# Performance work log

Hardware: AMD Instinct MI355X
Metric: run time of the kernel (lower is better)

Reference implementation:

```python
import jax, jax.numpy as jnp
import numpy as np


def setup_inputs() -> dict:
    key = jax.random.key(0)
    k1, k2 = jax.random.split(key)
    x = jax.random.normal(k1, (32, 128, 128, 128), dtype=jnp.float32)
    conv_w = jax.random.normal(k2, (1, 2, 7, 7), dtype=jnp.float32) * 0.1
    return {"x": x, "conv_w": conv_w}


def reference(x, conv_w):
    # x: [B, C, H, W]; conv_w: [1, 2, 7, 7]
    max_out = jnp.max(x, axis=1, keepdims=True)   # [B,1,H,W]
    avg_out = jnp.mean(x, axis=1, keepdims=True)  # [B,1,H,W]
    stacked = jnp.concatenate([avg_out, max_out], axis=1)  # [B,2,H,W]
    attn = jax.lax.conv_general_dilated(
        stacked, conv_w,
        window_strides=(1, 1), padding=((3, 3), (3, 3)),
        dimension_numbers=("NCHW", "OIHW", "NCHW"),
    )  # [B,1,H,W]
    return x * jax.nn.sigmoid(attn)
```

## Files before the change

kernel.cpp:

```cpp
#include <hip/hip_runtime.h>

#define BB 32
#define CC 128
#define HH 128
#define WW 128
#define HWSZ (HH * WW)
#define CHW (CC * HWSZ)
#define S4 (HWSZ / 4)
#define RPB 8
#define HALO 14

typedef float vfloat4 __attribute__((ext_vector_type(4)));

__device__ __forceinline__ vfloat4 fmax4(vfloat4 a, vfloat4 b) {
    vfloat4 r;
    r.x = fmaxf(a.x, b.x);
    r.y = fmaxf(a.y, b.y);
    r.z = fmaxf(a.z, b.z);
    r.w = fmaxf(a.w, b.w);
    return r;
}

__global__ __launch_bounds__(256, 2) void sa_onepass(
    const float* __restrict__ x, const float* __restrict__ cw,
    float* __restrict__ out) {
    __shared__ float m_lds[2][HALO][WW];
    __shared__ float sig_lds[RPB][WW];
    __shared__ float wsh[2 * 49];

    const int tid = threadIdx.x;
    const int wg  = blockIdx.x;
    const int xcd = wg & 7;
    const int lin = wg >> 3;
    const int b   = xcd * 4 + (lin >> 4);
    const int hb  = lin & 15;
    const int h0  = hb * RPB;

    if (tid < 98) wsh[tid] = cw[tid];

    const int r0 = tid >> 5;
    const int w4 = tid & 31;
    const float* xb = x + (size_t)b * CHW;

    const bool actB = (r0 < HALO - 8);
    const int gh_a = h0 - 3 + r0;
    const int gh_b = h0 - 3 + r0 + 8;
    const bool okA = (gh_a >= 0) && (gh_a < HH);
    const bool okB = actB && (gh_b < HH);
    const int cha = gh_a < 0 ? 0 : (gh_a > HH - 1 ? HH - 1 : gh_a);
    const int chb = gh_b > HH - 1 ? HH - 1 : gh_b;

    const vfloat4* pA = (const vfloat4*)(xb + cha * WW) + w4;
    const vfloat4* pB = (const vfloat4*)(xb + chb * WW) + w4;

    vfloat4 sumA, mxA;
    {
        vfloat4 v = pA[0];
        sumA = v; mxA = v;
    }
    #pragma unroll 8
    for (int c = 1; c < CC; ++c) {
        vfloat4 v = pA[(size_t)c * S4];
        sumA += v;
        mxA = fmax4(mxA, v);
    }
    vfloat4 sumB = {0.f, 0.f, 0.f, 0.f}, mxB = sumB;
    if (actB) {
        vfloat4 v = pB[0];
        sumB = v; mxB = v;
        #pragma unroll 8
        for (int c = 1; c < CC; ++c) {
            vfloat4 t = pB[(size_t)c * S4];
            sumB += t;
            mxB = fmax4(mxB, t);
        }
    }

    const float invC = 1.0f / (float)CC;
    {
        vfloat4 avgA = sumA * invC;
        if (!okA) { avgA = (vfloat4){0,0,0,0}; mxA = (vfloat4){0,0,0,0}; }
        *(vfloat4*)&m_lds[0][r0][w4 * 4] = avgA;
        *(vfloat4*)&m_lds[1][r0][w4 * 4] = mxA;
        if (actB) {
            vfloat4 avgB = sumB * invC;
            if (!okB) { avgB = (vfloat4){0,0,0,0}; mxB = (vfloat4){0,0,0,0}; }
            *(vfloat4*)&m_lds[0][r0 + 8][w4 * 4] = avgB;
            *(vfloat4*)&m_lds[1][r0 + 8][w4 * 4] = mxB;
        }
    }
    __syncthreads();

    {
        const int q = tid >> 7;
        const int w = tid & 127;
        float attn[4] = {0.f, 0.f, 0.f, 0.f};
        #pragma unroll
        for (int ic = 0; ic < 2; ++ic) {
            #pragma unroll
            for (int L = 0; L < 10; ++L) {
                const float* row = &m_lds[ic][q * 4 + L][0];
                #pragma unroll
                for (int kw = 0; kw < 7; ++kw) {
                    int wi = w - 3 + kw;
                    float v = (wi >= 0 && wi < WW) ? row[wi] : 0.0f;
                    #pragma unroll
                    for (int j = 0; j < 4; ++j) {
                        const int kh = L - j;
                        if (kh >= 0 && kh <= 6)
                            attn[j] = fmaf(v, wsh[ic * 49 + kh * 7 + kw], attn[j]);
                    }
                }
            }
        }
        #pragma unroll
        for (int j = 0; j < 4; ++j)
            sig_lds[q * 4 + j][w] = 1.0f / (1.0f + __expf(-attn[j]));
    }
    __syncthreads();

    {
        vfloat4 sig = *(const vfloat4*)&sig_lds[r0][w4 * 4];
        const int s = (h0 + r0) * WW + w4 * 4;
        const vfloat4* px = (const vfloat4*)xb + (s >> 2);
        vfloat4* po = (vfloat4*)(out + (size_t)b * CHW) + (s >> 2);
        #pragma unroll 1
        for (int c0 = CC - 8; c0 >= 0; c0 -= 8) {
            vfloat4 v[8];
            #pragma unroll
            for (int j = 0; j < 8; ++j)
                v[j] = px[(size_t)(c0 + 7 - j) * S4];
            #pragma unroll
            for (int j = 0; j < 8; ++j) {
                vfloat4 o = v[j] * sig;
                __builtin_nontemporal_store(o, po + (size_t)(c0 + 7 - j) * S4);
            }
        }
    }
}

extern "C" void kernel_launch(void* const* d_in, const int* in_sizes, int n_in,
                              void* d_out, int out_size, void* d_ws, size_t ws_size,
                              hipStream_t stream) {
    const float* x  = (const float*)d_in[0];
    const float* cw = (const float*)d_in[1];
    float* out = (float*)d_out;

    sa_onepass<<<BB * (HH / RPB), 256, 0, stream>>>(x, cw, out);
}
```

Baseline: 141.1 us.

## Split fused kernel into reduce-conv kernel and grid-stride multiply kernel

Splits the single-pass kernel into two. The first computes the channel mean/max, runs the 7x7 conv and writes the sigmoid map to workspace. The second is a flat grid-stride kernel that multiplies x by the broadcast sigmoid map, iterating in reverse order so it can reuse x still in cache. This trades the fused design's locality for better occupancy and parallelism in the multiply phase, at the cost of an extra launch, a workspace round trip and re-reading x from memory.

```diff
diff --git a/kernel.cpp b/kernel.cpp
--- a/kernel.cpp
+++ b/kernel.cpp
@@ -21,11 +21,10 @@
     return r;
 }
 
-__global__ __launch_bounds__(256, 2) void sa_onepass(
+__global__ __launch_bounds__(256, 2) void kA_reduce_conv(
     const float* __restrict__ x, const float* __restrict__ cw,
-    float* __restrict__ out) {
+    float* __restrict__ sig) {
     __shared__ float m_lds[2][HALO][WW];
-    __shared__ float sig_lds[RPB][WW];
     __shared__ float wsh[2 * 49];
 
     const int tid = threadIdx.x;
@@ -114,28 +113,25 @@
             }
         }
         #pragma unroll
-        for (int j = 0; j < 4; ++j)
-            sig_lds[q * 4 + j][w] = 1.0f / (1.0f + __expf(-attn[j]));
+        for (int j = 0; j < 4; ++j) {
+            float sv = 1.0f / (1.0f + __expf(-attn[j]));
+            sig[(size_t)b * HWSZ + (h0 + q * 4 + j) * WW + w] = sv;
+        }
     }
-    __syncthreads();
+}
 
-    {
-        vfloat4 sig = *(const vfloat4*)&sig_lds[r0][w4 * 4];
-        const int s = (h0 + r0) * WW + w4 * 4;
-        const vfloat4* px = (const vfloat4*)xb + (s >> 2);
-        vfloat4* po = (vfloat4*)(out + (size_t)b * CHW) + (s >> 2);
-        #pragma unroll 1
-        for (int c0 = CC - 8; c0 >= 0; c0 -= 8) {
-            vfloat4 v[8];
-            #pragma unroll
-            for (int j = 0; j < 8; ++j)
-                v[j] = px[(size_t)(c0 + 7 - j) * S4];
-            #pragma unroll
-            for (int j = 0; j < 8; ++j) {
-                vfloat4 o = v[j] * sig;
-                __builtin_nontemporal_store(o, po + (size_t)(c0 + 7 - j) * S4);
-            }
-        }
+__global__ __launch_bounds__(256) void kB_mul(
+    const float* __restrict__ x, const float* __restrict__ sig,
+    float* __restrict__ out) {
+    const int TOT4 = BB * CC * HWSZ / 4;
+    int stride = gridDim.x * blockDim.x;
+    for (int j = blockIdx.x * blockDim.x + threadIdx.x; j < TOT4; j += stride) {
+        int i = TOT4 - 1 - j;
+        int b = i >> 19;
+        int s4 = i & (S4 - 1);
+        vfloat4 xv = __builtin_nontemporal_load(reinterpret_cast<const vfloat4*>(x) + (size_t)i);
+        vfloat4 sv = reinterpret_cast<const vfloat4*>(sig)[(size_t)b * S4 + s4];
+        __builtin_nontemporal_store(xv * sv, reinterpret_cast<vfloat4*>(out) + (size_t)i);
     }
 }
 
@@ -145,6 +141,8 @@
     const float* x  = (const float*)d_in[0];
     const float* cw = (const float*)d_in[1];
     float* out = (float*)d_out;
+    float* sig = (float*)d_ws;
 
-    sa_onepass<<<BB * (HH / RPB), 256, 0, stream>>>(x, cw, out);
+    kA_reduce_conv<<<BB * (HH / RPB), 256, 0, stream>>>(x, cw, sig);
+    kB_mul<<<8192, 256, 0, stream>>>(x, sig, out);
 }
```

Result: slower. 155.5 us (+10.2%).
